# Performance work log

Hardware: AMD Instinct MI355X
Metric: run time of the kernel (lower is better)

Reference implementation:

```python
import jax, jax.numpy as jnp
import numpy as np

NUM_ROUTING = 3


def squash(s, axis):
    # v = |s|^2/(1+|s|^2) * s/|s|  (eq. 1 of the CapsNet paper)
    mag_sq = jnp.sum(s * s, axis=axis, keepdims=True)
    mag = jnp.sqrt(mag_sq)
    return mag_sq / (1.0 + mag_sq) * (s / mag)


def setup_inputs() -> dict:
    key = jax.random.key(0)
    k1, k2 = jax.random.split(key)
    B, I, C, U, S = 256, 8, 1152, 10, 16
    x = jax.random.normal(k1, (B, I, C), dtype=jnp.float32)
    weight = jax.random.normal(k2, (1, C, U, S, I), dtype=jnp.float32)
    return {"x": x, "weight": weight}


def reference(x, weight):
    # x: [B, in_unit, in_channel]; weight: [1, C, U, S, I]
    B = x.shape[0]
    C, U = weight.shape[1], weight.shape[2]
    x_t = jnp.transpose(x, (0, 2, 1))  # [B, C, I]
    # u_hat[b,c,u,s] = sum_i W[0,c,u,s,i] * x_t[b,c,i]
    u_hat = jnp.einsum('cusi,bci->bcus', weight[0], x_t)  # [B, C, U, S]

    b_ij = jnp.zeros((1, C, U, 1), dtype=u_hat.dtype)
    # s_j = (c_ij * u_hat).sum(dim=0): c_ij is batch-independent, so
    # precompute the batch-sum once instead of re-broadcasting each iter.
    u_sum = jnp.sum(u_hat, axis=0, keepdims=True)  # [1, C, U, S]

    v_j = None
    for _ in range(NUM_ROUTING):
        c_ij = jax.nn.softmax(b_ij, axis=2)          # [1, C, U, 1]
        s_j = c_ij * u_sum                           # [1, C, U, S]
        v_j = squash(s_j, axis=3)                    # [1, C, U, S]
        # agreement: mean over batch of <u_hat[b,c,u,:], v_j[0,c,u,:]>
        u_vj1 = jnp.einsum('bcus,cus->cu', u_hat, v_j[0]) / B  # [C, U]
        b_ij = b_ij + u_vj1[None, :, :, None]
    return v_j[0]  # squeeze -> [C, U, S]
```

## Files before the change

### kernel.cpp

```cpp
#include <hip/hip_runtime.h>

#define B_DIM 256
#define I_DIM 8
#define C_DIM 1152
#define U_DIM 10
#define S_DIM 16
#define T_DIM (I_DIM * C_DIM)
#define NCHUNK 8

__global__ __launch_bounds__(256) void batch_reduce_kernel(
    const float* __restrict__ x, float* __restrict__ partial) {
    const int t = blockIdx.x * 256 + threadIdx.x;
    const int k = blockIdx.y;
    const float* p = x + (size_t)(k * (B_DIM / NCHUNK)) * T_DIM + t;
    float acc = 0.f;
#pragma unroll
    for (int b = 0; b < B_DIM / NCHUNK; ++b)
        acc += p[(size_t)b * T_DIM];
    partial[k * T_DIM + t] = acc;
}

__global__ __launch_bounds__(64) void routing_kernel(
    const float* __restrict__ partial, const float* __restrict__ W,
    float* __restrict__ out) {
    __shared__ float foldbuf[2][32];
    __shared__ float xs_lds[32];

    const int tid = threadIdx.x;
    const int c0 = blockIdx.x * 4;

    {
        const int p = tid & 31;
        const int grp = tid >> 5;
        const int c_l = p >> 3, ii = p & 7;
        const float* pp = partial + (size_t)grp * 4 * T_DIM + ii * C_DIM + (c0 + c_l);
        float a = 0.f;
#pragma unroll
        for (int k = 0; k < 4; ++k) a += pp[(size_t)k * T_DIM];
        foldbuf[grp][p] = a;
    }
    __syncthreads();
    if (tid < 32) xs_lds[tid] = foldbuf[0][tid] + foldbuf[1][tid];
    __syncthreads();

    const int c_local = tid >> 4;
    const int s = tid & 15;
    const int c = c0 + c_local;

    float xs[I_DIM];
#pragma unroll
    for (int i = 0; i < I_DIM; ++i) xs[i] = xs_lds[c_local * 8 + i];

    float us[U_DIM];
#pragma unroll
    for (int u = 0; u < U_DIM; ++u) {
        const float4* w = (const float4*)(W + (((size_t)c * U_DIM + u) * S_DIM + s) * I_DIM);
        float4 w0 = w[0], w1 = w[1];
        us[u] = w0.x * xs[0] + w0.y * xs[1] + w0.z * xs[2] + w0.w * xs[3] +
                w1.x * xs[4] + w1.y * xs[5] + w1.z * xs[6] + w1.w * xs[7];
    }

    float bij[U_DIM];
    float v[U_DIM];

#pragma unroll
    for (int u = 0; u < U_DIM; ++u) {
        const float sj = 0.1f * us[u];
        float msq = sj * sj;
#pragma unroll
        for (int w = 1; w < 16; w <<= 1) msq += __shfl_xor(msq, w);
        const float vv = (msq / (1.f + msq)) * (sj * __frsqrt_rn(msq) * rsqrtf(msq) * msq) ;
        (void)vv;
        const float mag = sqrtf(msq);
        const float v0 = (msq / (1.f + msq)) * (sj / mag);
        v[u] = v0;
        float a = us[u] * v0;
#pragma unroll
        for (int w = 1; w < 16; w <<= 1) a += __shfl_xor(a, w);
        bij[u] = a * (1.f / (float)B_DIM);
    }

#pragma unroll
    for (int it = 1; it < 3; ++it) {
        float m = bij[0];
#pragma unroll
        for (int u = 1; u < U_DIM; ++u) m = fmaxf(m, bij[u]);
        float e[U_DIM];
        float sum = 0.f;
#pragma unroll
        for (int u = 0; u < U_DIM; ++u) { e[u] = __expf(bij[u] - m); sum += e[u]; }
        const float inv = 1.f / sum;

#pragma unroll
        for (int u = 0; u < U_DIM; ++u) {
            const float sj = e[u] * inv * us[u];
            float msq = sj * sj;
#pragma unroll
            for (int w = 1; w < 16; w <<= 1) msq += __shfl_xor(msq, w);
            const float mag = sqrtf(msq);
            const float vv = (msq / (1.f + msq)) * (sj / mag);
            v[u] = vv;
            if (it < 2) {
                float a = us[u] * vv;
#pragma unroll
                for (int w = 1; w < 16; w <<= 1) a += __shfl_xor(a, w);
                bij[u] += a * (1.f / (float)B_DIM);
            }
        }
    }

#pragma unroll
    for (int u = 0; u < U_DIM; ++u)
        out[(size_t)c * (U_DIM * S_DIM) + u * S_DIM + s] = v[u];
}

extern "C" void kernel_launch(void* const* d_in, const int* in_sizes, int n_in,
                              void* d_out, int out_size, void* d_ws, size_t ws_size,
                              hipStream_t stream) {
    const float* x = (const float*)d_in[0];
    const float* W = (const float*)d_in[1];
    float* out = (float*)d_out;
    float* partial = (float*)d_ws;

    dim3 g1(T_DIM / 256, NCHUNK);
    batch_reduce_kernel<<<g1, 256, 0, stream>>>(x, partial);

    routing_kernel<<<C_DIM / 4, 64, 0, stream>>>(partial, W, out);
}
```

Baseline: 72.30 us.

## Fuse batch reduction of x into routing kernel, dropping partial workspace

```diff
diff --git a/kernel.cpp b/kernel.cpp
--- a/kernel.cpp
+++ b/kernel.cpp
@@ -5,51 +5,54 @@
 #define C_DIM 1152
 #define U_DIM 10
 #define S_DIM 16
-#define T_DIM (I_DIM * C_DIM)
-#define NCHUNK 8
+#define ROWS  (B_DIM * I_DIM)
+#define CPB   4
+#define TPB   128
 
-__global__ __launch_bounds__(256) void batch_reduce_kernel(
-    const float* __restrict__ x, float* __restrict__ partial) {
-    const int t = blockIdx.x * 256 + threadIdx.x;
-    const int k = blockIdx.y;
-    const float* p = x + (size_t)(k * (B_DIM / NCHUNK)) * T_DIM + t;
-    float acc = 0.f;
+__global__ __launch_bounds__(TPB) void capsule_fused_kernel(
+    const float* __restrict__ x, const float* __restrict__ W,
+    float* __restrict__ out) {
+    __shared__ float red[2][I_DIM][CPB];
+    __shared__ float xs_lds[I_DIM][CPB];
+
+    const int t = threadIdx.x;
+    const int lane = t & 63;
+    const int wv = t >> 6;
+    const int c0 = blockIdx.x * CPB;
+
+    float4 acc = make_float4(0.f, 0.f, 0.f, 0.f);
+    const float* px = x + (size_t)t * C_DIM + c0;
 #pragma unroll
-    for (int b = 0; b < B_DIM / NCHUNK; ++b)
-        acc += p[(size_t)b * T_DIM];
-    partial[k * T_DIM + t] = acc;
-}
-
-__global__ __launch_bounds__(64) void routing_kernel(
-    const float* __restrict__ partial, const float* __restrict__ W,
-    float* __restrict__ out) {
-    __shared__ float foldbuf[2][32];
-    __shared__ float xs_lds[32];
-
-    const int tid = threadIdx.x;
-    const int c0 = blockIdx.x * 4;
-
-    {
-        const int p = tid & 31;
-        const int grp = tid >> 5;
-        const int c_l = p >> 3, ii = p & 7;
-        const float* pp = partial + (size_t)grp * 4 * T_DIM + ii * C_DIM + (c0 + c_l);
-        float a = 0.f;
+    for (int k = 0; k < ROWS / TPB; ++k) {
+        float4 v = *(const float4*)(px + (size_t)k * TPB * C_DIM);
+        acc.x += v.x; acc.y += v.y; acc.z += v.z; acc.w += v.w;
+    }
 #pragma unroll
-        for (int k = 0; k < 4; ++k) a += pp[(size_t)k * T_DIM];
-        foldbuf[grp][p] = a;
+    for (int m = 8; m <= 32; m <<= 1) {
+        acc.x += __shfl_xor(acc.x, m);
+        acc.y += __shfl_xor(acc.y, m);
+        acc.z += __shfl_xor(acc.z, m);
+        acc.w += __shfl_xor(acc.w, m);
+    }
+    if (lane < I_DIM) {
+        red[wv][lane][0] = acc.x; red[wv][lane][1] = acc.y;
+        red[wv][lane][2] = acc.z; red[wv][lane][3] = acc.w;
     }
     __syncthreads();
-    if (tid < 32) xs_lds[tid] = foldbuf[0][tid] + foldbuf[1][tid];
+    if (t < I_DIM * CPB) {
+        const int i = t >> 2, col = t & 3;
+        xs_lds[i][col] = red[0][i][col] + red[1][i][col];
+    }
     __syncthreads();
+    if (t >= 64) return;
 
-    const int c_local = tid >> 4;
-    const int s = tid & 15;
+    const int c_local = t >> 4;
+    const int s = t & 15;
     const int c = c0 + c_local;
 
     float xs[I_DIM];
 #pragma unroll
-    for (int i = 0; i < I_DIM; ++i) xs[i] = xs_lds[c_local * 8 + i];
+    for (int i = 0; i < I_DIM; ++i) xs[i] = xs_lds[i][c_local];
 
     float us[U_DIM];
 #pragma unroll
@@ -69,8 +72,6 @@
         float msq = sj * sj;
 #pragma unroll
         for (int w = 1; w < 16; w <<= 1) msq += __shfl_xor(msq, w);
-        const float vv = (msq / (1.f + msq)) * (sj * __frsqrt_rn(msq) * rsqrtf(msq) * msq) ;
-        (void)vv;
         const float mag = sqrtf(msq);
         const float v0 = (msq / (1.f + msq)) * (sj / mag);
         v[u] = v0;
@@ -120,10 +121,6 @@
     const float* x = (const float*)d_in[0];
     const float* W = (const float*)d_in[1];
     float* out = (float*)d_out;
-    float* partial = (float*)d_ws;
 
-    dim3 g1(T_DIM / 256, NCHUNK);
-    batch_reduce_kernel<<<g1, 256, 0, stream>>>(x, partial);
-
-    routing_kernel<<<C_DIM / 4, 64, 0, stream>>>(partial, W, out);
+    capsule_fused_kernel<<<C_DIM / CPB, TPB, 0, stream>>>(x, W, out);
 }
```

After: 81.08 us. +12.1%, slower.
